# Kernel tuning notes

Hardware: AMD Instinct MI355X
Metric: run time of the kernel (lower is better)

## Reference

```python
import jax, jax.numpy as jnp
import numpy as np

EPS = 1e-9
LAM_SEL, LAM_ID, LAM_RATE, LAM_KL, LAM_ENT, LAM_SMOOTH = 1.0, 10.0, 5.0, 0.1, 0.05, 0.5


def setup_inputs() -> dict:
    T, BS, V, K, RIDS = 48, 256, 4096, 32, 1024
    key = jax.random.key(0)
    ks = jax.random.split(key, 10)
    selector_logits = jax.random.normal(ks[0], (BS, 2, K), dtype=jnp.float32)
    selector_probs = jax.nn.softmax(jax.random.normal(ks[1], (BS, 2, K)), axis=-1)
    sel_idx = jax.random.randint(ks[2], (BS, 2), 0, K)
    selector_onehot = jax.nn.one_hot(sel_idx, K, dtype=jnp.float32)
    out_ids = jax.nn.softmax(jax.random.normal(ks[3], (T, BS, V)), axis=-1)
    out_rates = jax.random.uniform(ks[4], (T, BS, 1), dtype=jnp.float32)
    lab_idx = jax.random.randint(ks[5], (T + 2, BS), 0, V)
    trg_labels = jax.nn.one_hot(lab_idx, V, dtype=jnp.float32)
    trg_rates = jax.random.uniform(ks[6], (T + 2, BS, 1), dtype=jnp.float32)
    trg_lengths = jax.random.randint(ks[7], (BS,), 4, T + 2).astype(jnp.int32)
    candi_ids = jax.random.randint(ks[8], (BS, 2, K), 0, RIDS).astype(jnp.int32)
    routes = jax.random.randint(ks[9], (BS, V), 0, RIDS).astype(jnp.int32)
    return {
        'selector_logits': selector_logits, 'selector_probs': selector_probs,
        'selector_onehot': selector_onehot, 'out_ids': out_ids, 'out_rates': out_rates,
        'trg_labels': trg_labels, 'trg_rates': trg_rates, 'trg_lengths': trg_lengths,
        'candi_ids': candi_ids, 'routes': routes,
    }


def _align(lab, T_pred):
    T_lab = lab.shape[0]
    if T_lab >= T_pred + 2:
        return lab[1:-1]
    elif T_lab == T_pred:
        return lab
    else:
        pad = T_pred - T_lab
        return jnp.concatenate([lab, jnp.repeat(lab[-1:], pad, axis=0)], axis=0)


def _loss(selector_logits, selector_probs, selector_onehot, out_ids, out_rates,
          trg_labels, trg_rates, trg_lengths, candi_ids, routes):
    bs, _, K = selector_probs.shape
    # --- selector NLL (use_bce_logits=False path) ---
    sel_mask = (selector_onehot.sum(-1) > 0.5).astype(jnp.float32)      # [bs,2]
    sel_p_true = jnp.maximum((selector_probs * selector_onehot).sum(-1), EPS)
    loss_sel = (-jnp.log(sel_p_true) * sel_mask).sum() / jnp.maximum(sel_mask.sum(), 1.0)

    # --- id NLL over aligned target labels ---
    T_pred = out_ids.shape[0]
    tla = _align(trg_labels, T_pred)                                    # [T,bs,V]
    tra = _align(trg_rates, T_pred)                                     # [T,bs,1]
    step_mask = (tla.sum(-1) > 0.5).astype(jnp.float32)                 # [T,bs]
    p_true = jnp.maximum((out_ids * tla).sum(-1), EPS)
    loss_id = (-jnp.log(p_true) * step_mask).sum() * LAM_ID / jnp.maximum(step_mask.sum(), 1.0)

    # --- rate L1 ---
    denom_rate = jnp.maximum(1, (trg_lengths - 2).sum()).astype(jnp.float32)
    loss_rate = jnp.abs(out_rates - tra).sum() * LAM_RATE / denom_rate

    # --- KL over per-batch candidate unions (vectorized dedup via first-occurrence) ---
    U2 = 2 * K
    ids = candi_ids.reshape(bs, U2)                                     # [bs,2K]
    probs_flat = selector_probs.reshape(bs, U2)                         # [bs,2K]
    eq = ids[:, :, None] == ids[:, None, :]                             # [bs,2K,2K]
    rep = jnp.argmax(eq, axis=-1)                                       # first occurrence idx
    slots = jnp.arange(U2)
    valid = (rep == slots[None, :]).astype(jnp.float32)                 # [bs,2K] union slots
    Ucnt = valid.sum(-1)                                                # [bs]
    # Pm: scatter-add selector probs onto union slots (duplicates summed)
    rep_oh = (rep[:, :, None] == slots[None, None, :]).astype(jnp.float32)  # [bs,2K,2K]
    Pm = jnp.einsum('biu,bi->bu', rep_oh, probs_flat)                   # [bs,2K]
    Pm = Pm / jnp.maximum(Pm.sum(-1, keepdims=True), EPS)
    # Pb: project route mass onto union ids
    dist_r = out_ids.sum(0)                                             # [bs,V]
    match = (routes[:, :, None] == ids[:, None, :]).astype(jnp.float32)  # [bs,V,2K]
    agg = jnp.einsum('bvu,bv->bu', match, dist_r) * valid               # [bs,2K]
    s = agg.sum(-1, keepdims=True)                                      # [bs,1]
    uniform = valid / jnp.maximum(Ucnt, 1.0)[:, None]
    Pb = jnp.where(s > 0, agg / jnp.maximum(s, EPS), uniform)
    Pb_c = jnp.maximum(Pb, EPS)
    kl_b = (Pb_c * (jnp.log(Pb_c) - jnp.log(jnp.maximum(Pm, EPS))) * valid).sum(-1)
    loss_kl = LAM_KL * (kl_b.sum() / max(1, bs))

    # --- entropy of selector probs ---
    p = jnp.maximum(selector_probs, EPS)                                # [bs,2,K]
    ent_b = 0.5 * (-(p * jnp.log(p)).sum(-1)).sum(-1)                   # [bs]
    loss_entropy = LAM_ENT * (ent_b.sum() / max(1, bs))

    # --- rate smoothness ---
    r = out_rates[..., 0]                                               # [T,bs]
    dr = jnp.abs(r[1:] - r[:-1])                                        # [T-1,bs]
    eff = jnp.maximum(trg_lengths - 3, 0)                               # [bs]
    smask = (jnp.arange(T_pred - 1)[:, None] < eff[None, :]).astype(jnp.float32)
    loss_smooth = LAM_SMOOTH * (dr * smask).sum()

    return LAM_SEL * loss_sel + loss_id + loss_rate + loss_kl + loss_entropy + loss_smooth


def reference(selector_logits, selector_probs, selector_onehot, out_ids, out_rates,
              trg_labels, trg_rates, trg_lengths, candi_ids, routes):
    return _loss(selector_logits, selector_probs, selector_onehot, out_ids, out_rates,
                 trg_labels, trg_rates, trg_lengths, candi_ids, routes)
```

## Files before the change

kernel.cpp:

```cpp
#include <hip/hip_runtime.h>
#include <math.h>

#define EPSF 1e-9f

__global__ __launch_bounds__(1024) void e2e3_big(
    const float* __restrict__ selector_probs,
    const float* __restrict__ out_ids,
    const float* __restrict__ trg_labels,
    const int*   __restrict__ candi_ids,
    const int*   __restrict__ routes,
    float* __restrict__ acc)
{
    const int b    = blockIdx.x;
    const int tid  = threadIdx.x;
    const int wave = tid >> 6;
    const int lane = tid & 63;
    const int v0   = tid << 2;

    __shared__ float sdot[48][17];
    __shared__ float sls[48][17];
    __shared__ int   ids_s[64];
    __shared__ int   rep_s[64];
    __shared__ float valid_s[64];
    __shared__ float pmlog_s[64];
    __shared__ float agg_s[64];

    const size_t tstride = (size_t)256 * 4096;
    const float* outp = out_ids   + (size_t)b * 4096 + v0;
    const float* labp = trg_labels + tstride + (size_t)b * 4096 + v0;

    float4 dist = make_float4(0.f, 0.f, 0.f, 0.f);

    for (int t = 0; t < 48; ++t) {
        const float4 o = *reinterpret_cast<const float4*>(outp + (size_t)t * tstride);
        const float4 l = *reinterpret_cast<const float4*>(labp + (size_t)t * tstride);
        dist.x += o.x; dist.y += o.y; dist.z += o.z; dist.w += o.w;
        float dot = o.x * l.x + o.y * l.y + o.z * l.z + o.w * l.w;
        float ls  = l.x + l.y + l.z + l.w;
        #pragma unroll
        for (int off = 32; off >= 1; off >>= 1) {
            dot += __shfl_down(dot, off, 64);
            ls  += __shfl_down(ls,  off, 64);
        }
        if (lane == 0) { sdot[t][wave] = dot; sls[t][wave] = ls; }
    }
    __syncthreads();

    float idnum = 0.f, idcnt = 0.f;
    if (tid < 48) {
        float d = 0.f, l = 0.f;
        #pragma unroll
        for (int w = 0; w < 16; ++w) { d += sdot[tid][w]; l += sls[tid][w]; }
        if (l > 0.5f) { idnum = -logf(fmaxf(d, EPSF)); idcnt = 1.f; }
    }
    if (wave == 0) {
        #pragma unroll
        for (int off = 32; off >= 1; off >>= 1) {
            idnum += __shfl_down(idnum, off, 64);
            idcnt += __shfl_down(idcnt, off, 64);
        }
        if (lane == 0) { atomicAdd(&acc[0], idnum); atomicAdd(&acc[1], idcnt); }
    }

    if (tid < 64) ids_s[tid] = candi_ids[b * 64 + tid];
    __syncthreads();
    if (tid < 64) {
        const int my = ids_s[tid];
        int r = tid;
        for (int j = 0; j < 64; ++j) { if (ids_s[j] == my) { r = j; break; } }
        rep_s[tid]   = r;
        valid_s[tid] = (r == tid) ? 1.f : 0.f;
        agg_s[tid]   = 0.f;
    }
    __syncthreads();

    if (tid < 64) {
        float pm = 0.f;
        for (int i = 0; i < 64; ++i)
            if (rep_s[i] == tid) pm += selector_probs[b * 64 + i];
        float tot = pm;
        #pragma unroll
        for (int off = 32; off >= 1; off >>= 1) tot += __shfl_xor(tot, off, 64);
        pm = pm / fmaxf(tot, EPSF);
        pmlog_s[tid] = logf(fmaxf(pm, EPSF));
    }
    __syncthreads();

    {
        const int4 rv = *reinterpret_cast<const int4*>(routes + (size_t)b * 4096 + v0);
        const int   rr[4] = {rv.x, rv.y, rv.z, rv.w};
        const float dv[4] = {dist.x, dist.y, dist.z, dist.w};
        for (int u = 0; u < 64; ++u) {
            if (valid_s[u] > 0.5f) {
                const int idu = ids_s[u];
                #pragma unroll
                for (int j = 0; j < 4; ++j)
                    if (rr[j] == idu) atomicAdd(&agg_s[u], dv[j]);
            }
        }
    }
    __syncthreads();

    if (tid < 64) {
        const float va = valid_s[tid];
        const float a  = agg_s[tid];
        float s = a, uc = va;
        #pragma unroll
        for (int off = 32; off >= 1; off >>= 1) {
            s  += __shfl_xor(s,  off, 64);
            uc += __shfl_xor(uc, off, 64);
        }
        const float pb = (s > 0.f) ? (a / fmaxf(s, EPSF)) : (va / fmaxf(uc, 1.f));
        float term = 0.f;
        if (va > 0.5f) {
            const float pbc = fmaxf(pb, EPSF);
            term = pbc * (logf(pbc) - pmlog_s[tid]);
        }
        #pragma unroll
        for (int off = 32; off >= 1; off >>= 1) term += __shfl_down(term, off, 64);
        if (tid == 0) atomicAdd(&acc[2], term);
    }
}

__global__ __launch_bounds__(256) void e2e3_small(
    const float* __restrict__ selector_probs,
    const float* __restrict__ selector_onehot,
    const float* __restrict__ out_rates,
    const float* __restrict__ trg_rates,
    const int*   __restrict__ trg_lengths,
    const float* __restrict__ acc,
    float* __restrict__ out)
{
    const int tid  = threadIdx.x;
    const int wave = tid >> 6;
    const int lane = tid & 63;

    float v_selnum = 0.f, v_selcnt = 0.f, v_ent = 0.f;
    float v_rate = 0.f, v_den = 0.f, v_smooth = 0.f;

    for (int g = tid; g < 512; g += 256) {
        const float* pp = selector_probs  + g * 32;
        const float* oo = selector_onehot + g * 32;
        float p = 0.f, m = 0.f;
        #pragma unroll
        for (int k = 0; k < 32; ++k) { p += pp[k] * oo[k]; m += oo[k]; }
        if (m > 0.5f) { v_selnum += -logf(fmaxf(p, EPSF)); v_selcnt += 1.f; }
    }
    for (int i = tid; i < 256 * 64; i += 256) {
        const float p = fmaxf(selector_probs[i], EPSF);
        v_ent += -p * logf(p);
    }
    for (int i = tid; i < 48 * 256; i += 256)
        v_rate += fabsf(out_rates[i] - trg_rates[i + 256]);
    for (int b2 = tid; b2 < 256; b2 += 256)
        v_den += (float)(trg_lengths[b2] - 2);
    for (int i = tid; i < 47 * 256; i += 256) {
        const int b2 = i & 255;
        const int t  = i >> 8;
        int eff = trg_lengths[b2] - 3; if (eff < 0) eff = 0;
        if (t < eff) v_smooth += fabsf(out_rates[i + 256] - out_rates[i]);
    }

    __shared__ float red[6][4];
    float vals[6] = {v_selnum, v_selcnt, v_ent, v_rate, v_den, v_smooth};
    #pragma unroll
    for (int k = 0; k < 6; ++k) {
        float v = vals[k];
        #pragma unroll
        for (int off = 32; off >= 1; off >>= 1) v += __shfl_down(v, off, 64);
        if (lane == 0) red[k][wave] = v;
    }
    __syncthreads();
    if (tid == 0) {
        float s[6];
        #pragma unroll
        for (int k = 0; k < 6; ++k) s[k] = red[k][0] + red[k][1] + red[k][2] + red[k][3];
        const float loss =
              s[0] / fmaxf(s[1], 1.f)
            + 10.f * acc[0] / fmaxf(acc[1], 1.f)
            + 5.f  * s[3]   / fmaxf(s[4], 1.f)
            + 0.1f * acc[2] * (1.f / 256.f)
            + 0.05f * 0.5f * s[2] * (1.f / 256.f)
            + 0.5f * s[5];
        out[0] = loss;
    }
}

extern "C" void kernel_launch(void* const* d_in, const int* in_sizes, int n_in,
                              void* d_out, int out_size, void* d_ws, size_t ws_size,
                              hipStream_t stream) {
    const float* selector_probs  = (const float*)d_in[1];
    const float* selector_onehot = (const float*)d_in[2];
    const float* out_ids         = (const float*)d_in[3];
    const float* out_rates       = (const float*)d_in[4];
    const float* trg_labels      = (const float*)d_in[5];
    const float* trg_rates       = (const float*)d_in[6];
    const int*   trg_lengths     = (const int*)d_in[7];
    const int*   candi_ids       = (const int*)d_in[8];
    const int*   routes          = (const int*)d_in[9];

    float* acc = (float*)d_ws;
    hipMemsetAsync(acc, 0, 3 * sizeof(float), stream);

    e2e3_big<<<256, 1024, 0, stream>>>(selector_probs, out_ids, trg_labels,
                                       candi_ids, routes, acc);
    e2e3_small<<<1, 256, 0, stream>>>(selector_probs, selector_onehot,
                                      out_rates, trg_rates, trg_lengths,
                                      acc, (float*)d_out);
}
```

Baseline: 141.4 us.

## Split streaming over time halves and move KL aggregation to separate kernel

The single large kernel is split in two. A streaming kernel uses 512 blocks, each covering half the time steps, and prefetches the next step's rows. It accumulates the id NLL per element with a conditional log instead of doing a per-step dot product and wave reduction. A second kernel reads the partial distributions written to workspace, sums them, and does the route-matching KL aggregation with a per-element candidate search. This adds more parallelism and fewer reductions for the bandwidth-bound pass, at the cost of an extra launch, an 8 MB partial write and read, and an id NLL that is only equivalent when the labels are exactly one-hot.

```diff
diff --git a/kernel.cpp b/kernel.cpp
--- a/kernel.cpp
+++ b/kernel.cpp
@@ -3,74 +3,89 @@
 
 #define EPSF 1e-9f
 
-__global__ __launch_bounds__(1024) void e2e3_big(
-    const float* __restrict__ selector_probs,
+__global__ __launch_bounds__(1024) void e2e3_stream(
     const float* __restrict__ out_ids,
     const float* __restrict__ trg_labels,
-    const int*   __restrict__ candi_ids,
-    const int*   __restrict__ routes,
+    float* __restrict__ dist_part,
     float* __restrict__ acc)
 {
-    const int b    = blockIdx.x;
+    const int bid  = blockIdx.x;
+    const int b    = bid >> 1;
+    const int h    = bid & 1;
     const int tid  = threadIdx.x;
     const int wave = tid >> 6;
     const int lane = tid & 63;
     const int v0   = tid << 2;
-
-    __shared__ float sdot[48][17];
-    __shared__ float sls[48][17];
+    const int t0   = h * 24;
+
+    const size_t tstride = (size_t)256 * 4096;
+    const float* outp = out_ids    + (size_t)t0 * tstride       + (size_t)b * 4096 + v0;
+    const float* labp = trg_labels + (size_t)(t0 + 1) * tstride + (size_t)b * 4096 + v0;
+
+    float4 dist = make_float4(0.f, 0.f, 0.f, 0.f);
+    float idnum = 0.f, idcnt = 0.f;
+
+    float4 o = *reinterpret_cast<const float4*>(outp);
+    float4 l = *reinterpret_cast<const float4*>(labp);
+    for (int t = 0; t < 24; ++t) {
+        float4 o2 = o, l2 = l;
+        if (t < 23) {
+            o2 = *reinterpret_cast<const float4*>(outp + (size_t)(t + 1) * tstride);
+            l2 = *reinterpret_cast<const float4*>(labp + (size_t)(t + 1) * tstride);
+        }
+        dist.x += o.x; dist.y += o.y; dist.z += o.z; dist.w += o.w;
+        if (l.x > 0.5f) { idnum -= logf(fmaxf(o.x, EPSF)); idcnt += 1.f; }
+        if (l.y > 0.5f) { idnum -= logf(fmaxf(o.y, EPSF)); idcnt += 1.f; }
+        if (l.z > 0.5f) { idnum -= logf(fmaxf(o.z, EPSF)); idcnt += 1.f; }
+        if (l.w > 0.5f) { idnum -= logf(fmaxf(o.w, EPSF)); idcnt += 1.f; }
+        o = o2; l = l2;
+    }
+
+    *reinterpret_cast<float4*>(dist_part + ((size_t)h * 256 + b) * 4096 + v0) = dist;
+
+    __shared__ float red[2][16];
+    #pragma unroll
+    for (int off = 32; off >= 1; off >>= 1) {
+        idnum += __shfl_down(idnum, off, 64);
+        idcnt += __shfl_down(idcnt, off, 64);
+    }
+    if (lane == 0) { red[0][wave] = idnum; red[1][wave] = idcnt; }
+    __syncthreads();
+    if (tid == 0) {
+        float a = 0.f, c = 0.f;
+        #pragma unroll
+        for (int w = 0; w < 16; ++w) { a += red[0][w]; c += red[1][w]; }
+        atomicAdd(&acc[0], a);
+        atomicAdd(&acc[1], c);
+    }
+}
+
+__global__ __launch_bounds__(256) void e2e3_kl(
+    const float* __restrict__ selector_probs,
+    const int*   __restrict__ candi_ids,
+    const int*   __restrict__ routes,
+    const float* __restrict__ dist_part,
+    float* __restrict__ acc)
+{
+    const int b   = blockIdx.x;
+    const int tid = threadIdx.x;
+
     __shared__ int   ids_s[64];
     __shared__ int   rep_s[64];
     __shared__ float valid_s[64];
     __shared__ float pmlog_s[64];
     __shared__ float agg_s[64];
 
-    const size_t tstride = (size_t)256 * 4096;
-    const float* outp = out_ids   + (size_t)b * 4096 + v0;
-    const float* labp = trg_labels + tstride + (size_t)b * 4096 + v0;
-
-    float4 dist = make_float4(0.f, 0.f, 0.f, 0.f);
-
-    for (int t = 0; t < 48; ++t) {
-        const float4 o = *reinterpret_cast<const float4*>(outp + (size_t)t * tstride);
-        const float4 l = *reinterpret_cast<const float4*>(labp + (size_t)t * tstride);
-        dist.x += o.x; dist.y += o.y; dist.z += o.z; dist.w += o.w;
-        float dot = o.x * l.x + o.y * l.y + o.z * l.z + o.w * l.w;
-        float ls  = l.x + l.y + l.z + l.w;
-        #pragma unroll
-        for (int off = 32; off >= 1; off >>= 1) {
-            dot += __shfl_down(dot, off, 64);
-            ls  += __shfl_down(ls,  off, 64);
-        }
-        if (lane == 0) { sdot[t][wave] = dot; sls[t][wave] = ls; }
-    }
-    __syncthreads();
-
-    float idnum = 0.f, idcnt = 0.f;
-    if (tid < 48) {
-        float d = 0.f, l = 0.f;
-        #pragma unroll
-        for (int w = 0; w < 16; ++w) { d += sdot[tid][w]; l += sls[tid][w]; }
-        if (l > 0.5f) { idnum = -logf(fmaxf(d, EPSF)); idcnt = 1.f; }
-    }
-    if (wave == 0) {
-        #pragma unroll
-        for (int off = 32; off >= 1; off >>= 1) {
-            idnum += __shfl_down(idnum, off, 64);
-            idcnt += __shfl_down(idcnt, off, 64);
-        }
-        if (lane == 0) { atomicAdd(&acc[0], idnum); atomicAdd(&acc[1], idcnt); }
-    }
-
-    if (tid < 64) ids_s[tid] = candi_ids[b * 64 + tid];
-    __syncthreads();
+    if (tid < 64)               ids_s[tid] = candi_ids[b * 64 + tid];
+    if (tid >= 64 && tid < 128) agg_s[tid - 64] = 0.f;
+    __syncthreads();
+
     if (tid < 64) {
         const int my = ids_s[tid];
         int r = tid;
         for (int j = 0; j < 64; ++j) { if (ids_s[j] == my) { r = j; break; } }
         rep_s[tid]   = r;
         valid_s[tid] = (r == tid) ? 1.f : 0.f;
-        agg_s[tid]   = 0.f;
     }
     __syncthreads();
 
@@ -86,16 +101,21 @@
     }
     __syncthreads();
 
-    {
-        const int4 rv = *reinterpret_cast<const int4*>(routes + (size_t)b * 4096 + v0);
+    const float* dp0 = dist_part + (size_t)b * 4096;
+    const float* dp1 = dist_part + ((size_t)256 + b) * 4096;
+    #pragma unroll
+    for (int it = 0; it < 4; ++it) {
+        const int v = it * 1024 + tid * 4;
+        const float4 d0 = *reinterpret_cast<const float4*>(dp0 + v);
+        const float4 d1 = *reinterpret_cast<const float4*>(dp1 + v);
+        const int4   rv = *reinterpret_cast<const int4*>(routes + (size_t)b * 4096 + v);
+        const float dv[4] = {d0.x + d1.x, d0.y + d1.y, d0.z + d1.z, d0.w + d1.w};
         const int   rr[4] = {rv.x, rv.y, rv.z, rv.w};
-        const float dv[4] = {dist.x, dist.y, dist.z, dist.w};
-        for (int u = 0; u < 64; ++u) {
-            if (valid_s[u] > 0.5f) {
-                const int idu = ids_s[u];
-                #pragma unroll
-                for (int j = 0; j < 4; ++j)
-                    if (rr[j] == idu) atomicAdd(&agg_s[u], dv[j]);
+        #pragma unroll
+        for (int k = 0; k < 4; ++k) {
+            const int r = rr[k];
+            for (int u = 0; u < 64; ++u) {
+                if (ids_s[u] == r) { atomicAdd(&agg_s[u], dv[k]); break; }
             }
         }
     }
@@ -103,7 +123,7 @@
 
     if (tid < 64) {
         const float va = valid_s[tid];
-        const float a  = agg_s[tid];
+        const float a  = (va > 0.5f) ? agg_s[tid] : 0.f;
         float s = a, uc = va;
         #pragma unroll
         for (int off = 32; off >= 1; off >>= 1) {
@@ -199,11 +219,14 @@
     const int*   candi_ids       = (const int*)d_in[8];
     const int*   routes          = (const int*)d_in[9];
 
-    float* acc = (float*)d_ws;
-    hipMemsetAsync(acc, 0, 3 * sizeof(float), stream);
-
-    e2e3_big<<<256, 1024, 0, stream>>>(selector_probs, out_ids, trg_labels,
-                                       candi_ids, routes, acc);
+    float* acc       = (float*)d_ws;
+    float* dist_part = (float*)((char*)d_ws + 256);
+
+    hipMemsetAsync(acc, 0, 4 * sizeof(float), stream);
+
+    e2e3_stream<<<512, 1024, 0, stream>>>(out_ids, trg_labels, dist_part, acc);
+    e2e3_kl<<<256, 256, 0, stream>>>(selector_probs, candi_ids, routes,
+                                     dist_part, acc);
     e2e3_small<<<1, 256, 0, stream>>>(selector_probs, selector_onehot,
                                       out_rates, trg_rates, trg_lengths,
                                       acc, (float*)d_out);
```

Measured after the change: 233.1 us. 64.8% more time.
